# Kernel tuning notes

Measured on AMD Instinct MI355X. Metric: run time of the kernel, lower is better.

## Reference

```python
import jax, jax.numpy as jnp
import numpy as np

EPS = 1e-6
REP = 28  # hardcoded expand factor in the original module: bs = 28 * time_stamp


def setup_inputs() -> dict:
    key = jax.random.key(0)
    k1, k2, k3, k4, k5 = jax.random.split(key, 5)
    T, N, E0, E1, IN_FT, OUT_FT = 8, 1024, 256, 256, 64, 64
    bs = REP * T
    x = jax.random.normal(k1, (bs, N, IN_FT), dtype=jnp.float32)
    G = jax.random.uniform(k2, (N, E0), dtype=jnp.float32)
    G1 = jax.random.uniform(k3, (T, N, E1), dtype=jnp.float32)
    stdv = 1.0 / np.sqrt(OUT_FT)
    weight = jax.random.uniform(k4, (IN_FT, OUT_FT), dtype=jnp.float32, minval=-stdv, maxval=stdv)
    bias = jax.random.uniform(k5, (OUT_FT,), dtype=jnp.float32, minval=-stdv, maxval=stdv)
    return {"x": x, "G": G, "G1": G1, "weight": weight, "bias": bias}


def reference(x, G, G1, weight, bias):
    T, N, _ = G1.shape
    bs = x.shape[0]
    # G_combined: static incidence broadcast over time, concat with dynamic part -> [T, N, E]
    Gc = jnp.concatenate([jnp.broadcast_to(G[None], (T,) + G.shape), G1], axis=-1)
    # Diagonal degree matrices -> just vectors; inv(sqrt(Dv)) and inv(De) are elementwise.
    dv_inv_sqrt = 1.0 / jnp.sqrt(Gc.sum(axis=2) + EPS)   # [T, N]
    de_inv = 1.0 / (Gc.sum(axis=1) + EPS)                # [T, E]
    # L = Dv^{-1/2} G De^{-1} G^T Dv^{-1/2}  -> [T, N, N]
    A = Gc * de_inv[:, None, :]
    L = dv_inv_sqrt[:, :, None] * jnp.einsum('tne,tme->tnm', A, Gc) * dv_inv_sqrt[:, None, :]
    # x @ W + b, then apply per-timestep Laplacian (each L repeated REP times along batch)
    xw = x @ weight + bias                                # [bs, N, F]
    F = xw.shape[-1]
    xw_t = xw.reshape(T, bs // T, N, F)
    out = jnp.einsum('tnm,tbmf->tbnf', L, xw_t).reshape(bs, N, F)
    return out
```

## Files before the change

kernel.cpp:

```cpp
#include <hip/hip_runtime.h>
#include <hip/hip_bf16.h>
#include <stdint.h>

typedef __bf16 bf16x8 __attribute__((ext_vector_type(8)));
typedef float f32x4 __attribute__((ext_vector_type(4)));
typedef unsigned short u16;

#define EPS_ 1e-6f

__device__ __forceinline__ void gload16(const void* g, void* l) {
  __builtin_amdgcn_global_load_lds((const __attribute__((address_space(1))) void*)g,
                                   (__attribute__((address_space(3))) void*)l,
                                   16, 0, 0);
}

__device__ __forceinline__ u16 f2bf(float v) {
  __hip_bfloat16 h = __float2bfloat16(v);
  return *reinterpret_cast<u16*>(&h);
}

__global__ void dv_kernel(const float* __restrict__ G, const float* __restrict__ G1,
                          float* __restrict__ dv) {
  const int row = blockIdx.x * 4 + (threadIdx.x >> 6);
  const int lane = threadIdx.x & 63;
  const int t = row >> 10, n = row & 1023;
  const float4 g  = ((const float4*)(G  + (size_t)n * 256))[lane];
  const float4 g1 = ((const float4*)(G1 + ((size_t)t * 1024 + n) * 256))[lane];
  float s = g.x + g.y + g.z + g.w + g1.x + g1.y + g1.z + g1.w;
  #pragma unroll
  for (int off = 1; off < 64; off <<= 1) s += __shfl_xor(s, off);
  if (lane == 0) dv[row] = rsqrtf(s + EPS_);
}

__global__ void de_partial_kernel(const float* __restrict__ G, const float* __restrict__ G1,
                                  float* __restrict__ dep) {
  const int t = blockIdx.x >> 4;
  const int c = blockIdx.x & 15;
  const int e = threadIdx.x;
  const int n0 = c * 64;
  float s = 0.0f;
  if (e < 256) {
    const float* p = G + (size_t)n0 * 256 + e;
    #pragma unroll 8
    for (int n = 0; n < 64; ++n) s += p[(size_t)n * 256];
  } else {
    const float* p = G1 + ((size_t)t * 1024 + n0) * 256 + (e - 256);
    #pragma unroll 8
    for (int n = 0; n < 64; ++n) s += p[(size_t)n * 256];
  }
  dep[(size_t)blockIdx.x * 512 + e] = s;
}

__global__ void de_final_kernel(const float* __restrict__ dep, float* __restrict__ de) {
  const int t = blockIdx.x;
  const int e = threadIdx.x;
  float s = 0.0f;
  #pragma unroll
  for (int c = 0; c < 16; ++c) s += dep[(size_t)(t * 16 + c) * 512 + e];
  de[t * 512 + e] = rsqrtf(s + EPS_);
}

__global__ void pack_kernel(const float* __restrict__ G, const float* __restrict__ G1,
                            const float* __restrict__ dv, const float* __restrict__ de,
                            u16* __restrict__ P) {
  const int idx = blockIdx.x * 256 + threadIdx.x;
  const int e4 = idx & 127;
  const int n  = (idx >> 7) & 1023;
  const int t  = idx >> 17;
  const int e  = e4 * 4;
  float4 g;
  if (e < 256) g = *(const float4*)(G + (size_t)n * 256 + e);
  else         g = *(const float4*)(G1 + ((size_t)t * 1024 + n) * 256 + (e - 256));
  const float4 d = *(const float4*)(de + t * 512 + e);
  const float dvn = dv[t * 1024 + n];
  u16 o[4];
  o[0] = f2bf(g.x * d.x * dvn);
  o[1] = f2bf(g.y * d.y * dvn);
  o[2] = f2bf(g.z * d.z * dvn);
  o[3] = f2bf(g.w * d.w * dvn);
  *(ushort4*)(P + ((size_t)t * 1024 + n) * 512 + e) = *(ushort4*)o;
}

__global__ __launch_bounds__(256) void xwt_mfma_kernel(
    const float* __restrict__ x, const float* __restrict__ w,
    const float* __restrict__ bias, u16* __restrict__ xt) {
  __shared__ u16 As[256 * 72];
  __shared__ u16 WT[64 * 136];
  const int tid = threadIdx.x;
  const int tb = blockIdx.x >> 2;
  const int m0 = (blockIdx.x & 3) * 256;
  const size_t r0 = (size_t)tb * 1024 + m0;

  {
    const int f = tid & 63, kq = tid >> 6;
    #pragma unroll
    for (int kk = 0; kk < 16; ++kk) {
      const int k = kq * 16 + kk;
      const float wv = w[k * 64 + f];
      const float hf = __bfloat162float(__float2bfloat16(wv));
      WT[f * 136 + k]      = f2bf(wv);
      WT[f * 136 + 64 + k] = f2bf(wv - hf);
    }
  }
  {
    const float4* xb = (const float4*)(x + r0 * 64);
    #pragma unroll
    for (int i = 0; i < 16; ++i) {
      const int fi = tid + i * 256;
      const int row = fi >> 4, c4 = fi & 15;
      const float4 v = xb[fi];
      ushort4 o = { f2bf(v.x), f2bf(v.y), f2bf(v.z), f2bf(v.w) };
      *(ushort4*)&As[row * 72 + c4 * 4] = o;
    }
  }
  __syncthreads();

  const int lane = tid & 63, wv_ = tid >> 6;
  const int c = lane & 15, q = lane >> 4;

  bf16x8 a[4][2], bf_[4][4];
  #pragma unroll
  for (int i = 0; i < 4; ++i)
    #pragma unroll
    for (int s = 0; s < 2; ++s)
      a[i][s] = *(const bf16x8*)&As[(wv_ * 64 + i * 16 + c) * 72 + s * 32 + q * 8];
  #pragma unroll
  for (int j = 0; j < 4; ++j)
    #pragma unroll
    for (int s = 0; s < 4; ++s)
      bf_[j][s] = *(const bf16x8*)&WT[(j * 16 + c) * 136 + s * 32 + q * 8];

  f32x4 acc[4][4];
  #pragma unroll
  for (int j = 0; j < 4; ++j) {
    const float bv = bias[j * 16 + c];
    #pragma unroll
    for (int i = 0; i < 4; ++i) acc[i][j] = { bv, bv, bv, bv };
  }
  #pragma unroll
  for (int i = 0; i < 4; ++i)
    #pragma unroll
    for (int j = 0; j < 4; ++j) {
      acc[i][j] = __builtin_amdgcn_mfma_f32_16x16x32_bf16(a[i][0], bf_[j][0], acc[i][j], 0, 0, 0);
      acc[i][j] = __builtin_amdgcn_mfma_f32_16x16x32_bf16(a[i][1], bf_[j][1], acc[i][j], 0, 0, 0);
      acc[i][j] = __builtin_amdgcn_mfma_f32_16x16x32_bf16(a[i][0], bf_[j][2], acc[i][j], 0, 0, 0);
      acc[i][j] = __builtin_amdgcn_mfma_f32_16x16x32_bf16(a[i][1], bf_[j][3], acc[i][j], 0, 0, 0);
    }

  u16* xtb = xt + (size_t)tb * 64 * 1024 + m0;
  #pragma unroll
  for (int j = 0; j < 4; ++j) {
    const int f = j * 16 + c;
    #pragma unroll
    for (int i = 0; i < 4; ++i) {
      const int mr = wv_ * 64 + i * 16 + q * 4;
      ushort4 o = { f2bf(acc[i][j][0]), f2bf(acc[i][j][1]),
                    f2bf(acc[i][j][2]), f2bf(acc[i][j][3]) };
      *(ushort4*)&xtb[(size_t)f * 1024 + mr] = o;
    }
  }
}

template <int K, int MODE, int CHUNK>
__global__ __launch_bounds__(256) void gemm_bt_kernel(
    const u16* __restrict__ Abase, const u16* __restrict__ Bbase,
    u16* __restrict__ Lw, float* __restrict__ Oo) {
  const int wg = (blockIdx.x & 7) * CHUNK + (blockIdx.x >> 3);
  const int t = wg / CHUNK;
  const int bx = wg - t * CHUNK;
  const int row0 = (bx & 7) * 128;
  const int col0 = (bx >> 3) * 128;
  const size_t aoff = (MODE == 0) ? (size_t)t * 1024 * 512 : (size_t)t * 1024 * 1024;
  const size_t boff = (MODE == 0) ? (size_t)t * 1024 * 512 : (size_t)t * 1792 * 1024;
  const u16* A = Abase + aoff;
  const u16* B = Bbase + boff;

  __shared__ u16 As[128 * 64];
  __shared__ u16 Bs[128 * 64];

  const int tid = threadIdx.x;
  const int lane = tid & 63;
  const int wave = tid >> 6;
  const int wr = wave & 1, wc = wave >> 1;

  const int srow8 = tid >> 3;
  const int schunk = tid & 7;

  f32x4 acc[4][4] = {};

  const int l16 = lane & 15;
  const int q = lane >> 4;

  for (int kt = 0; kt < K / 64; ++kt) {
    const int kk0 = kt * 64;
    #pragma unroll
    for (int i = 0; i < 4; ++i) {
      const int row = i * 32 + srow8;
      const int csrc = schunk ^ (row & 7);
      gload16(A + (size_t)(row0 + row) * K + kk0 + csrc * 8, &As[row * 64 + schunk * 8]);
      gload16(B + (size_t)(col0 + row) * K + kk0 + csrc * 8, &Bs[row * 64 + schunk * 8]);
    }
    __syncthreads();

    bf16x8 af[4][2], bfr[4][2];
    #pragma unroll
    for (int i = 0; i < 4; ++i) {
      const int ar = wr * 64 + i * 16 + l16;
      const int br = wc * 64 + i * 16 + l16;
      #pragma unroll
      for (int h = 0; h < 2; ++h) {
        const int ca = (h * 4 + q) ^ (ar & 7);
        const int cb = (h * 4 + q) ^ (br & 7);
        af[i][h]  = *(const bf16x8*)&As[ar * 64 + ca * 8];
        bfr[i][h] = *(const bf16x8*)&Bs[br * 64 + cb * 8];
      }
    }
    #pragma unroll
    for (int i = 0; i < 4; ++i)
      #pragma unroll
      for (int j = 0; j < 4; ++j) {
        acc[i][j] = __builtin_amdgcn_mfma_f32_16x16x32_bf16(af[i][0], bfr[j][0], acc[i][j], 0, 0, 0);
        acc[i][j] = __builtin_amdgcn_mfma_f32_16x16x32_bf16(af[i][1], bfr[j][1], acc[i][j], 0, 0, 0);
      }
    __syncthreads();
  }

  const int l4 = q;
  if constexpr (MODE == 0) {
    u16* Lt = Lw + (size_t)t * 1024 * 1024;
    #pragma unroll
    for (int i = 0; i < 4; ++i) {
      const int rbase = row0 + wr * 64 + i * 16 + l4 * 4;
      #pragma unroll
      for (int j = 0; j < 4; ++j) {
        const int col = col0 + wc * 64 + j * 16 + l16;
        #pragma unroll
        for (int r = 0; r < 4; ++r)
          Lt[(size_t)(rbase + r) * 1024 + col] = f2bf(acc[i][j][r]);
      }
    }
  } else {
    #pragma unroll
    for (int j = 0; j < 4; ++j) {
      const int jg = col0 + wc * 64 + j * 16 + l16;
      float* Ot = Oo + (((size_t)t * 28 + (jg >> 6)) * 1024) * 64 + (jg & 63);
      #pragma unroll
      for (int i = 0; i < 4; ++i) {
        const int rbase = row0 + wr * 64 + i * 16 + l4 * 4;
        #pragma unroll
        for (int r = 0; r < 4; ++r)
          Ot[(size_t)(rbase + r) * 64] = acc[i][j][r];
      }
    }
  }
}

extern "C" void kernel_launch(void* const* d_in, const int* in_sizes, int n_in,
                              void* d_out, int out_size, void* d_ws, size_t ws_size,
                              hipStream_t stream) {
  const float* x  = (const float*)d_in[0];
  const float* G  = (const float*)d_in[1];
  const float* G1 = (const float*)d_in[2];
  const float* W  = (const float*)d_in[3];
  const float* Bi = (const float*)d_in[4];
  float* out = (float*)d_out;

  char* ws = (char*)d_ws;
  float* dv = (float*)ws;
  float* de = (float*)(ws + 32768);
  u16*   P  = (u16*)(ws + 49152);
  u16*   L  = (u16*)(ws + 49152 + 8388608);
  u16*   XT = (u16*)(ws + 49152 + 8388608 + 16777216);
  float* dep = (float*)L;

  dv_kernel<<<2048, 256, 0, stream>>>(G, G1, dv);
  de_partial_kernel<<<128, 512, 0, stream>>>(G, G1, dep);
  de_final_kernel<<<8, 512, 0, stream>>>(dep, de);
  pack_kernel<<<4096, 256, 0, stream>>>(G, G1, dv, de, P);
  gemm_bt_kernel<512, 0, 64><<<512, 256, 0, stream>>>(P, P, L, nullptr);
  xwt_mfma_kernel<<<896, 256, 0, stream>>>(x, W, Bi, XT);
  gemm_bt_kernel<1024, 1, 112><<<896, 256, 0, stream>>>(L, XT, nullptr, out);
}
```

Baseline: 190.0 us.

## Merge degree kernels and co-schedule pack with xW projection in one launch

```diff
diff --git a/kernel.cpp b/kernel.cpp
--- a/kernel.cpp
+++ b/kernel.cpp
@@ -19,144 +19,148 @@
   return *reinterpret_cast<u16*>(&h);
 }
 
-__global__ void dv_kernel(const float* __restrict__ G, const float* __restrict__ G1,
-                          float* __restrict__ dv) {
-  const int row = blockIdx.x * 4 + (threadIdx.x >> 6);
-  const int lane = threadIdx.x & 63;
-  const int t = row >> 10, n = row & 1023;
-  const float4 g  = ((const float4*)(G  + (size_t)n * 256))[lane];
-  const float4 g1 = ((const float4*)(G1 + ((size_t)t * 1024 + n) * 256))[lane];
-  float s = g.x + g.y + g.z + g.w + g1.x + g1.y + g1.z + g1.w;
-  #pragma unroll
-  for (int off = 1; off < 64; off <<= 1) s += __shfl_xor(s, off);
-  if (lane == 0) dv[row] = rsqrtf(s + EPS_);
-}
-
-__global__ void de_partial_kernel(const float* __restrict__ G, const float* __restrict__ G1,
-                                  float* __restrict__ dep) {
-  const int t = blockIdx.x >> 4;
-  const int c = blockIdx.x & 15;
-  const int e = threadIdx.x;
-  const int n0 = c * 64;
-  float s = 0.0f;
-  if (e < 256) {
-    const float* p = G + (size_t)n0 * 256 + e;
-    #pragma unroll 8
-    for (int n = 0; n < 64; ++n) s += p[(size_t)n * 256];
+__global__ __launch_bounds__(512) void deg_kernel(const float* __restrict__ G,
+                                                  const float* __restrict__ G1,
+                                                  float* __restrict__ dv,
+                                                  float* __restrict__ dep) {
+  const int tid = threadIdx.x;
+  if (blockIdx.x < 128) {
+    const int t = blockIdx.x >> 4, c = blockIdx.x & 15, e = tid, n0 = c * 64;
+    float s = 0.0f;
+    if (e < 256) {
+      const float* p = G + (size_t)n0 * 256 + e;
+      #pragma unroll 8
+      for (int n = 0; n < 64; ++n) s += p[(size_t)n * 256];
+    } else {
+      const float* p = G1 + ((size_t)t * 1024 + n0) * 256 + (e - 256);
+      #pragma unroll 8
+      for (int n = 0; n < 64; ++n) s += p[(size_t)n * 256];
+    }
+    dep[(size_t)blockIdx.x * 512 + e] = s;
   } else {
-    const float* p = G1 + ((size_t)t * 1024 + n0) * 256 + (e - 256);
-    #pragma unroll 8
-    for (int n = 0; n < 64; ++n) s += p[(size_t)n * 256];
-  }
-  dep[(size_t)blockIdx.x * 512 + e] = s;
-}
-
-__global__ void de_final_kernel(const float* __restrict__ dep, float* __restrict__ de) {
-  const int t = blockIdx.x;
-  const int e = threadIdx.x;
-  float s = 0.0f;
-  #pragma unroll
-  for (int c = 0; c < 16; ++c) s += dep[(size_t)(t * 16 + c) * 512 + e];
-  de[t * 512 + e] = rsqrtf(s + EPS_);
-}
-
-__global__ void pack_kernel(const float* __restrict__ G, const float* __restrict__ G1,
-                            const float* __restrict__ dv, const float* __restrict__ de,
-                            u16* __restrict__ P) {
-  const int idx = blockIdx.x * 256 + threadIdx.x;
-  const int e4 = idx & 127;
-  const int n  = (idx >> 7) & 1023;
-  const int t  = idx >> 17;
-  const int e  = e4 * 4;
-  float4 g;
-  if (e < 256) g = *(const float4*)(G + (size_t)n * 256 + e);
-  else         g = *(const float4*)(G1 + ((size_t)t * 1024 + n) * 256 + (e - 256));
-  const float4 d = *(const float4*)(de + t * 512 + e);
-  const float dvn = dv[t * 1024 + n];
-  u16 o[4];
-  o[0] = f2bf(g.x * d.x * dvn);
-  o[1] = f2bf(g.y * d.y * dvn);
-  o[2] = f2bf(g.z * d.z * dvn);
-  o[3] = f2bf(g.w * d.w * dvn);
-  *(ushort4*)(P + ((size_t)t * 1024 + n) * 512 + e) = *(ushort4*)o;
-}
-
-__global__ __launch_bounds__(256) void xwt_mfma_kernel(
+    const int row = (blockIdx.x - 128) * 8 + (tid >> 6);
+    const int lane = tid & 63;
+    const int t = row >> 10, n = row & 1023;
+    const float4 g  = ((const float4*)(G  + (size_t)n * 256))[lane];
+    const float4 g1 = ((const float4*)(G1 + ((size_t)t * 1024 + n) * 256))[lane];
+    float s = g.x + g.y + g.z + g.w + g1.x + g1.y + g1.z + g1.w;
+    #pragma unroll
+    for (int off = 1; off < 64; off <<= 1) s += __shfl_xor(s, off);
+    if (lane == 0) dv[row] = rsqrtf(s + EPS_);
+  }
+}
+
+__global__ __launch_bounds__(256) void packxwt_kernel(
     const float* __restrict__ x, const float* __restrict__ w,
-    const float* __restrict__ bias, u16* __restrict__ xt) {
-  __shared__ u16 As[256 * 72];
-  __shared__ u16 WT[64 * 136];
+    const float* __restrict__ bias,
+    const float* __restrict__ G, const float* __restrict__ G1,
+    const float* __restrict__ dv, const float* __restrict__ dep,
+    u16* __restrict__ xt, u16* __restrict__ P) {
+  __shared__ u16 smem[256 * 72 + 64 * 136];
   const int tid = threadIdx.x;
-  const int tb = blockIdx.x >> 2;
-  const int m0 = (blockIdx.x & 3) * 256;
-  const size_t r0 = (size_t)tb * 1024 + m0;
-
-  {
-    const int f = tid & 63, kq = tid >> 6;
-    #pragma unroll
-    for (int kk = 0; kk < 16; ++kk) {
-      const int k = kq * 16 + kk;
-      const float wv = w[k * 64 + f];
-      const float hf = __bfloat162float(__float2bfloat16(wv));
-      WT[f * 136 + k]      = f2bf(wv);
-      WT[f * 136 + 64 + k] = f2bf(wv - hf);
-    }
-  }
-  {
-    const float4* xb = (const float4*)(x + r0 * 64);
-    #pragma unroll
-    for (int i = 0; i < 16; ++i) {
-      const int fi = tid + i * 256;
-      const int row = fi >> 4, c4 = fi & 15;
-      const float4 v = xb[fi];
-      ushort4 o = { f2bf(v.x), f2bf(v.y), f2bf(v.z), f2bf(v.w) };
-      *(ushort4*)&As[row * 72 + c4 * 4] = o;
-    }
-  }
-  __syncthreads();
-
-  const int lane = tid & 63, wv_ = tid >> 6;
-  const int c = lane & 15, q = lane >> 4;
-
-  bf16x8 a[4][2], bf_[4][4];
-  #pragma unroll
-  for (int i = 0; i < 4; ++i)
-    #pragma unroll
-    for (int s = 0; s < 2; ++s)
-      a[i][s] = *(const bf16x8*)&As[(wv_ * 64 + i * 16 + c) * 72 + s * 32 + q * 8];
-  #pragma unroll
-  for (int j = 0; j < 4; ++j)
-    #pragma unroll
-    for (int s = 0; s < 4; ++s)
-      bf_[j][s] = *(const bf16x8*)&WT[(j * 16 + c) * 136 + s * 32 + q * 8];
-
-  f32x4 acc[4][4];
-  #pragma unroll
-  for (int j = 0; j < 4; ++j) {
-    const float bv = bias[j * 16 + c];
-    #pragma unroll
-    for (int i = 0; i < 4; ++i) acc[i][j] = { bv, bv, bv, bv };
-  }
-  #pragma unroll
-  for (int i = 0; i < 4; ++i)
+
+  if (blockIdx.x < 896) {
+    u16* As = smem;
+    u16* WT = smem + 256 * 72;
+    const int tb = blockIdx.x >> 2;
+    const int m0 = (blockIdx.x & 3) * 256;
+    const size_t r0 = (size_t)tb * 1024 + m0;
+
+    {
+      const int f = tid & 63, kq = tid >> 6;
+      #pragma unroll
+      for (int kk = 0; kk < 16; ++kk) {
+        const int k = kq * 16 + kk;
+        const float wv = w[k * 64 + f];
+        const float hf = __bfloat162float(__float2bfloat16(wv));
+        WT[f * 136 + k]      = f2bf(wv);
+        WT[f * 136 + 64 + k] = f2bf(wv - hf);
+      }
+    }
+    {
+      const float4* xb = (const float4*)(x + r0 * 64);
+      #pragma unroll
+      for (int i = 0; i < 16; ++i) {
+        const int fi = tid + i * 256;
+        const int row = fi >> 4, c4 = fi & 15;
+        const float4 v = xb[fi];
+        ushort4 o = { f2bf(v.x), f2bf(v.y), f2bf(v.z), f2bf(v.w) };
+        *(ushort4*)&As[row * 72 + c4 * 4] = o;
+      }
+    }
+    __syncthreads();
+
+    const int lane = tid & 63, wv_ = tid >> 6;
+    const int c = lane & 15, q = lane >> 4;
+
+    bf16x8 a[4][2], bf_[4][4];
+    #pragma unroll
+    for (int i = 0; i < 4; ++i)
+      #pragma unroll
+      for (int s = 0; s < 2; ++s)
+        a[i][s] = *(const bf16x8*)&As[(wv_ * 64 + i * 16 + c) * 72 + s * 32 + q * 8];
+    #pragma unroll
+    for (int j = 0; j < 4; ++j)
+      #pragma unroll
+      for (int s = 0; s < 4; ++s)
+        bf_[j][s] = *(const bf16x8*)&WT[(j * 16 + c) * 136 + s * 32 + q * 8];
+
+    f32x4 acc[4][4];
     #pragma unroll
     for (int j = 0; j < 4; ++j) {
-      acc[i][j] = __builtin_amdgcn_mfma_f32_16x16x32_bf16(a[i][0], bf_[j][0], acc[i][j], 0, 0, 0);
-      acc[i][j] = __builtin_amdgcn_mfma_f32_16x16x32_bf16(a[i][1], bf_[j][1], acc[i][j], 0, 0, 0);
-      acc[i][j] = __builtin_amdgcn_mfma_f32_16x16x32_bf16(a[i][0], bf_[j][2], acc[i][j], 0, 0, 0);
-      acc[i][j] = __builtin_amdgcn_mfma_f32_16x16x32_bf16(a[i][1], bf_[j][3], acc[i][j], 0, 0, 0);
-    }
-
-  u16* xtb = xt + (size_t)tb * 64 * 1024 + m0;
-  #pragma unroll
-  for (int j = 0; j < 4; ++j) {
-    const int f = j * 16 + c;
-    #pragma unroll
-    for (int i = 0; i < 4; ++i) {
-      const int mr = wv_ * 64 + i * 16 + q * 4;
-      ushort4 o = { f2bf(acc[i][j][0]), f2bf(acc[i][j][1]),
-                    f2bf(acc[i][j][2]), f2bf(acc[i][j][3]) };
-      *(ushort4*)&xtb[(size_t)f * 1024 + mr] = o;
+      const float bv = bias[j * 16 + c];
+      #pragma unroll
+      for (int i = 0; i < 4; ++i) acc[i][j] = { bv, bv, bv, bv };
+    }
+    #pragma unroll
+    for (int i = 0; i < 4; ++i)
+      #pragma unroll
+      for (int j = 0; j < 4; ++j) {
+        acc[i][j] = __builtin_amdgcn_mfma_f32_16x16x32_bf16(a[i][0], bf_[j][0], acc[i][j], 0, 0, 0);
+        acc[i][j] = __builtin_amdgcn_mfma_f32_16x16x32_bf16(a[i][1], bf_[j][1], acc[i][j], 0, 0, 0);
+        acc[i][j] = __builtin_amdgcn_mfma_f32_16x16x32_bf16(a[i][0], bf_[j][2], acc[i][j], 0, 0, 0);
+        acc[i][j] = __builtin_amdgcn_mfma_f32_16x16x32_bf16(a[i][1], bf_[j][3], acc[i][j], 0, 0, 0);
+      }
+
+    u16* xtb = xt + (size_t)tb * 64 * 1024 + m0;
+    #pragma unroll
+    for (int j = 0; j < 4; ++j) {
+      const int f = j * 16 + c;
+      #pragma unroll
+      for (int i = 0; i < 4; ++i) {
+        const int mr = wv_ * 64 + i * 16 + q * 4;
+        ushort4 o = { f2bf(acc[i][j][0]), f2bf(acc[i][j][1]),
+                      f2bf(acc[i][j][2]), f2bf(acc[i][j][3]) };
+        *(ushort4*)&xtb[(size_t)f * 1024 + mr] = o;
+      }
+    }
+  } else {
+    float* de_s = (float*)smem;
+    const int pb = blockIdx.x - 896;
+    const int t = pb >> 5;
+    const int n0 = (pb & 31) * 32;
+    for (int e = tid; e < 512; e += 256) {
+      float s = 0.0f;
+      #pragma unroll
+      for (int c = 0; c < 16; ++c) s += dep[(size_t)(t * 16 + c) * 512 + e];
+      de_s[e] = rsqrtf(s + EPS_);
+    }
+    __syncthreads();
+    const int e = (tid & 127) * 4;
+    const int rsub = tid >> 7;
+    #pragma unroll
+    for (int it = 0; it < 16; ++it) {
+      const int n = n0 + it * 2 + rsub;
+      float4 g;
+      if (e < 256) g = *(const float4*)(G + (size_t)n * 256 + e);
+      else         g = *(const float4*)(G1 + ((size_t)t * 1024 + n) * 256 + (e - 256));
+      const float dvn = dv[t * 1024 + n];
+      u16 o[4];
+      o[0] = f2bf(g.x * de_s[e]     * dvn);
+      o[1] = f2bf(g.y * de_s[e + 1] * dvn);
+      o[2] = f2bf(g.z * de_s[e + 2] * dvn);
+      o[3] = f2bf(g.w * de_s[e + 3] * dvn);
+      *(ushort4*)(P + ((size_t)t * 1024 + n) * 512 + e) = *(ushort4*)o;
     }
   }
 }
@@ -267,17 +271,13 @@
 
   char* ws = (char*)d_ws;
   float* dv = (float*)ws;
-  float* de = (float*)(ws + 32768);
   u16*   P  = (u16*)(ws + 49152);
   u16*   L  = (u16*)(ws + 49152 + 8388608);
   u16*   XT = (u16*)(ws + 49152 + 8388608 + 16777216);
   float* dep = (float*)L;
 
-  dv_kernel<<<2048, 256, 0, stream>>>(G, G1, dv);
-  de_partial_kernel<<<128, 512, 0, stream>>>(G, G1, dep);
-  de_final_kernel<<<8, 512, 0, stream>>>(dep, de);
-  pack_kernel<<<4096, 256, 0, stream>>>(G, G1, dv, de, P);
+  deg_kernel<<<1152, 512, 0, stream>>>(G, G1, dv, dep);
+  packxwt_kernel<<<1152, 256, 0, stream>>>(x, W, Bi, G, G1, dv, dep, XT, P);
   gemm_bt_kernel<512, 0, 64><<<512, 256, 0, stream>>>(P, P, L, nullptr);
-  xwt_mfma_kernel<<<896, 256, 0, stream>>>(x, W, Bi, XT);
   gemm_bt_kernel<1024, 1, 112><<<896, 256, 0, stream>>>(L, XT, nullptr, out);
 }
```

After: 183.8 us. 3.2% less time.
